# Kernel tuning notes

Hardware: AMD Instinct MI355X
Metric: run time of the kernel (lower is better)

Reference implementation:

```python
import jax, jax.numpy as jnp
import numpy as np

B = 4194304  # number of sequential rows


def setup_inputs() -> dict:
    key = jax.random.key(0)
    k1, k2, k3, k4 = jax.random.split(key, 4)
    x = jax.random.normal(k1, (B, 1, 3), dtype=jnp.float32)
    # nn.Linear(3, 3) params
    lim = 1.0 / np.sqrt(3.0)
    W = jax.random.uniform(k2, (3, 3), minval=-lim, maxval=lim, dtype=jnp.float32)
    b = jax.random.uniform(k3, (3,), minval=-lim, maxval=lim, dtype=jnp.float32)
    # FastNetwork init: (-1-1)*rand([3,1]) + 1  -> uniform in [-1, 1]
    net0 = jax.random.uniform(k4, (3, 1), minval=-1.0, maxval=1.0, dtype=jnp.float32)
    return {"x": x, "W": W, "b": b, "net0": net0}


def reference(x, W, b, net0):
    # x: [B,1,3]; W: [3,3]; b: [3]; net0: [3,1]
    xi = x[:, 0, :]                      # [B,3]
    # Updater: per-row Linear(3,3) -- batched as one matmul
    updates = xi @ W.T + b               # [B,3]

    def step(net, inp):
        x_row, u = inp                   # x_row: [3], u: [3]
        # 1/(1+exp(-10*(net + update - 0.5))) == sigmoid(10*(net + update - 0.5))
        net = jax.nn.sigmoid(10.0 * (net + u[:, None] - 0.5))  # [3,1]
        pred = x_row @ net               # [1]
        return net, pred

    _, preds = jax.lax.scan(step, net0, (xi, updates))
    return preds                         # [B,1]
```

## Files before the change

### kernel.cpp

```cpp
#include <hip/hip_runtime.h>


#if __has_builtin(__builtin_amdgcn_exp2f)
#define EXP2F(v) __builtin_amdgcn_exp2f(v)
#else
#define EXP2F(v) __expf(0.6931471805599453f * (v))
#endif

namespace {
constexpr int   BTOT   = 4194304;
constexpr int   CHUNK  = 16;
constexpr int   BLOCK  = 256;
constexpr int   BSTEPS = BLOCK * CHUNK;
constexpr int   WARM   = 32;
constexpr int   GRID   = BTOT / BSTEPS;
constexpr float KEXP   = -14.426950408889634f;
constexpr float EPS    = 1e-6f;
}

#define CVALS(X0, X1, X2)                                                     \
  const float c0 = fmaf(kw00, (X0), fmaf(kw01, (X1), fmaf(kw02, (X2), kb0)));  \
  const float c1 = fmaf(kw10, (X0), fmaf(kw11, (X1), fmaf(kw12, (X2), kb1)));  \
  const float c2 = fmaf(kw20, (X0), fmaf(kw21, (X1), fmaf(kw22, (X2), kb2)));

#define SIG(N, C) __builtin_amdgcn_rcpf(1.0f + EXP2F(fmaf(KEXP, (N), (C))))

#define US(X0, X1, X2)                                                        \
  do {                                                                        \
    CVALS(X0, X1, X2)                                                         \
    lo0 = SIG(lo0, c0); hi0 = SIG(hi0, c0);                                   \
    lo1 = SIG(lo1, c1); hi1 = SIG(hi1, c1);                                   \
    lo2 = SIG(lo2, c2); hi2 = SIG(hi2, c2);                                   \
  } while (0)

#define SS(X0, X1, X2)                                                        \
  do {                                                                        \
    CVALS(X0, X1, X2)                                                         \
    m0 = SIG(m0, c0); m1 = SIG(m1, c1); m2 = SIG(m2, c2);                     \
  } while (0)

#define MS(IDX, X0, X1, X2)                                                   \
  do {                                                                        \
    CVALS(X0, X1, X2)                                                         \
    m0 = SIG(m0, c0); m1 = SIG(m1, c1); m2 = SIG(m2, c2);                     \
    pr[(IDX)] = fmaf((X0), m0, fmaf((X1), m1, (X2) * m2));                    \
  } while (0)

__global__ __launch_bounds__(BLOCK, 4) void Updater_65395172049297_kernel(
    const float* __restrict__ x, const float* __restrict__ W,
    const float* __restrict__ bv, const float* __restrict__ n0v,
    float* __restrict__ out)
{
    const float kw00 = KEXP * W[0], kw01 = KEXP * W[1], kw02 = KEXP * W[2];
    const float kw10 = KEXP * W[3], kw11 = KEXP * W[4], kw12 = KEXP * W[5];
    const float kw20 = KEXP * W[6], kw21 = KEXP * W[7], kw22 = KEXP * W[8];
    const float kb0 = KEXP * (bv[0] - 0.5f);
    const float kb1 = KEXP * (bv[1] - 0.5f);
    const float kb2 = KEXP * (bv[2] - 0.5f);
    const float n00 = n0v[0], n01 = n0v[1], n02 = n0v[2];

    const long start = (long)blockIdx.x * BSTEPS + (long)threadIdx.x * CHUNK;
    const int  wl    = (int)((start < (long)WARM) ? start : (long)WARM);
    const bool exact = (start - wl) == 0;
    const int  gw    = wl >> 2;

    const float4* wp = reinterpret_cast<const float4*>(x + 3 * (start - wl));

    float lo0, lo1, lo2, hi0, hi1, hi2, m0, m1, m2;
    bool  conv = false;
    int   g    = 0;

    if (exact) {
        m0 = n00; m1 = n01; m2 = n02; conv = true;
    } else {
        lo0 = lo1 = lo2 = 0.0f; hi0 = hi1 = hi2 = 1.0f;
        float4 A = wp[0], B4 = wp[1], C4 = wp[2];
        while (g < gw) {
            const float4 An = wp[3 * g + 3], Bn = wp[3 * g + 4], Cn = wp[3 * g + 5];
            US(A.x, A.y, A.z);
            US(A.w, B4.x, B4.y);
            US(B4.z, B4.w, C4.x);
            US(C4.y, C4.z, C4.w);
            ++g;
            conv = ((hi0 - lo0) < EPS) & ((hi1 - lo1) < EPS) & ((hi2 - lo2) < EPS);
            if (__all(conv)) break;
            A = An; B4 = Bn; C4 = Cn;
        }
        if (conv) { m0 = 0.5f * (lo0 + hi0); m1 = 0.5f * (lo1 + hi1); m2 = 0.5f * (lo2 + hi2); }
    }

    if (conv) {
        for (; g < gw; ++g) {
            const float4 a4 = wp[3 * g], b4 = wp[3 * g + 1], c4 = wp[3 * g + 2];
            SS(a4.x, a4.y, a4.z);
            SS(a4.w, b4.x, b4.y);
            SS(b4.z, b4.w, c4.x);
            SS(c4.y, c4.z, c4.w);
        }
    } else {
        for (int at = 1; at < 10 && !conv; ++at) {
            long wl2 = (long)WARM << (2 * at);
            long bgn = start - wl2;
            bool ex2 = (bgn <= 0);
            if (ex2) bgn = 0;
            if (ex2) { lo0 = hi0 = n00; lo1 = hi1 = n01; lo2 = hi2 = n02; }
            else     { lo0 = lo1 = lo2 = 0.0f; hi0 = hi1 = hi2 = 1.0f; }
            const float4* bp = reinterpret_cast<const float4*>(x + 3 * bgn);
            const long ng = (start - bgn) >> 2;
            for (long q = 0; q < ng; ++q) {
                const float4 a4 = bp[3 * q], b4 = bp[3 * q + 1], c4 = bp[3 * q + 2];
                US(a4.x, a4.y, a4.z);
                US(a4.w, b4.x, b4.y);
                US(b4.z, b4.w, c4.x);
                US(c4.y, c4.z, c4.w);
            }
            conv = ex2 || (((hi0 - lo0) < EPS) & ((hi1 - lo1) < EPS) & ((hi2 - lo2) < EPS));
        }
        m0 = 0.5f * (lo0 + hi0); m1 = 0.5f * (lo1 + hi1); m2 = 0.5f * (lo2 + hi2);
    }

    const float4* mp = reinterpret_cast<const float4*>(x + 3 * start);
    float pr[CHUNK];
#pragma unroll
    for (int q = 0; q < CHUNK / 4; ++q) {
        const float4 a4 = mp[3 * q], b4 = mp[3 * q + 1], c4 = mp[3 * q + 2];
        MS(4 * q + 0, a4.x, a4.y, a4.z);
        MS(4 * q + 1, a4.w, b4.x, b4.y);
        MS(4 * q + 2, b4.z, b4.w, c4.x);
        MS(4 * q + 3, c4.y, c4.z, c4.w);
    }

    float4* op = reinterpret_cast<float4*>(out + start);
#pragma unroll
    for (int i = 0; i < CHUNK / 4; ++i)
        op[i] = make_float4(pr[4 * i + 0], pr[4 * i + 1], pr[4 * i + 2], pr[4 * i + 3]);
}

extern "C" void kernel_launch(void* const* d_in, const int* in_sizes, int n_in,
                              void* d_out, int out_size, void* d_ws, size_t ws_size,
                              hipStream_t stream) {
    const float* x   = (const float*)d_in[0];
    const float* W   = (const float*)d_in[1];
    const float* bv  = (const float*)d_in[2];
    const float* n0v = (const float*)d_in[3];
    float*       out = (float*)d_out;
    Updater_65395172049297_kernel<<<GRID, BLOCK, 0, stream>>>(x, W, bv, n0v, out);
}
```

Before: 117.4 us.

## Source warm-up rows from neighbor lanes via ds_bpermute instead of global reloads

Each thread now loads its own 16 rows once into registers. During the 32-step warm-up it pulls the preceding rows from lanes one or two positions lower using ds_bpermute, rather than re-reading the overlapping window from global memory. The first lanes of each wavefront, which have no lower neighbor, read their warm-up rows from a small shared-memory buffer filled before a block barrier. The main pass reuses the register copy of the rows, and the warm-up is fully unrolled with predication for the first wavefront. In exchange it adds register pressure from the 48-float array, cross-lane shuffles, a __syncthreads, and more complex unrolled control flow.

Measured after the change: 103.3 us. 12.0% less time.

```diff
diff --git a/kernel.cpp b/kernel.cpp
--- a/kernel.cpp
+++ b/kernel.cpp
@@ -18,39 +18,104 @@
 constexpr float EPS    = 1e-6f;
 }
 
-#define CVALS(X0, X1, X2)                                                     \
-  const float c0 = fmaf(kw00, (X0), fmaf(kw01, (X1), fmaf(kw02, (X2), kb0)));  \
-  const float c1 = fmaf(kw10, (X0), fmaf(kw11, (X1), fmaf(kw12, (X2), kb1)));  \
-  const float c2 = fmaf(kw20, (X0), fmaf(kw21, (X1), fmaf(kw22, (X2), kb2)));
+#define CVALS(X0_, X1_, X2_)                                                   \
+  const float c0 = fmaf(kw00, (X0_), fmaf(kw01, (X1_), fmaf(kw02, (X2_), kb0))); \
+  const float c1 = fmaf(kw10, (X0_), fmaf(kw11, (X1_), fmaf(kw12, (X2_), kb1))); \
+  const float c2 = fmaf(kw20, (X0_), fmaf(kw21, (X1_), fmaf(kw22, (X2_), kb2)));
 
 #define SIG(N, C) __builtin_amdgcn_rcpf(1.0f + EXP2F(fmaf(KEXP, (N), (C))))
 
-#define US(X0, X1, X2)                                                        \
-  do {                                                                        \
-    CVALS(X0, X1, X2)                                                         \
-    lo0 = SIG(lo0, c0); hi0 = SIG(hi0, c0);                                   \
-    lo1 = SIG(lo1, c1); hi1 = SIG(hi1, c1);                                   \
-    lo2 = SIG(lo2, c2); hi2 = SIG(hi2, c2);                                   \
+#define PULL(VAL_, AD_)                                                        \
+  __int_as_float(__builtin_amdgcn_ds_bpermute((AD_), __float_as_int(VAL_)))
+
+#define WSTEP_FETCH(S_)                                                        \
+  float X0, X1, X2;                                                            \
+  {                                                                            \
+    const int ad_ = ((S_) < 16) ? a2 : a1;                                     \
+    X0 = PULL(fx[3 * ((S_) & 15) + 0], ad_);                                   \
+    X1 = PULL(fx[3 * ((S_) & 15) + 1], ad_);                                   \
+    X2 = PULL(fx[3 * ((S_) & 15) + 2], ad_);                                   \
+    if (lane < (((S_) < 16) ? 2 : 1)) {                                        \
+      const float4 wv = wbuf[w][lane * 16 + (S_)];                             \
+      X0 = wv.x; X1 = wv.y; X2 = wv.z;                                         \
+    }                                                                          \
+  }
+
+#define WSTEP_DUAL(S_, PRED_)                                                  \
+  {                                                                            \
+    WSTEP_FETCH(S_)                                                            \
+    CVALS(X0, X1, X2)                                                          \
+    const float a0_ = SIG(lo0, c0), b0_ = SIG(hi0, c0);                        \
+    const float a1_ = SIG(lo1, c1), b1_ = SIG(hi1, c1);                        \
+    const float a2_ = SIG(lo2, c2), b2_ = SIG(hi2, c2);                        \
+    if (PRED_) {                                                               \
+      const bool kp_ = (S_) >= smin;                                           \
+      lo0 = kp_ ? a0_ : lo0; hi0 = kp_ ? b0_ : hi0;                            \
+      lo1 = kp_ ? a1_ : lo1; hi1 = kp_ ? b1_ : hi1;                            \
+      lo2 = kp_ ? a2_ : lo2; hi2 = kp_ ? b2_ : hi2;                            \
+    } else {                                                                   \
+      lo0 = a0_; hi0 = b0_; lo1 = a1_; hi1 = b1_; lo2 = a2_; hi2 = b2_;        \
+    }                                                                          \
+  }
+
+#define WSTEP_SNG(S_, PRED_)                                                   \
+  {                                                                            \
+    WSTEP_FETCH(S_)                                                            \
+    CVALS(X0, X1, X2)                                                          \
+    const float t0_ = SIG(m0, c0), t1_ = SIG(m1, c1), t2_ = SIG(m2, c2);       \
+    if (PRED_) {                                                               \
+      const bool kp_ = (S_) >= smin;                                           \
+      m0 = kp_ ? t0_ : m0; m1 = kp_ ? t1_ : m1; m2 = kp_ ? t2_ : m2;           \
+    } else {                                                                   \
+      m0 = t0_; m1 = t1_; m2 = t2_;                                            \
+    }                                                                          \
+  }
+
+#define WARM_GROUP(G_, PRED_)                                                  \
+  if (!single) {                                                               \
+    WSTEP_DUAL(4 * (G_) + 0, PRED_)                                            \
+    WSTEP_DUAL(4 * (G_) + 1, PRED_)                                            \
+    WSTEP_DUAL(4 * (G_) + 2, PRED_)                                            \
+    WSTEP_DUAL(4 * (G_) + 3, PRED_)                                            \
+    conv = ((hi0 - lo0) < EPS) & ((hi1 - lo1) < EPS) & ((hi2 - lo2) < EPS);    \
+    if (__all(conv)) {                                                         \
+      m0 = 0.5f * (lo0 + hi0); m1 = 0.5f * (lo1 + hi1); m2 = 0.5f * (lo2 + hi2); \
+      single = true;                                                           \
+    }                                                                          \
+  } else {                                                                     \
+    WSTEP_SNG(4 * (G_) + 0, PRED_)                                             \
+    WSTEP_SNG(4 * (G_) + 1, PRED_)                                             \
+    WSTEP_SNG(4 * (G_) + 2, PRED_)                                             \
+    WSTEP_SNG(4 * (G_) + 3, PRED_)                                             \
+  }
+
+#define WARM_ALL(PRED_)                                                        \
+  WARM_GROUP(0, PRED_) WARM_GROUP(1, PRED_) WARM_GROUP(2, PRED_)               \
+  WARM_GROUP(3, PRED_) WARM_GROUP(4, PRED_) WARM_GROUP(5, PRED_)               \
+  WARM_GROUP(6, PRED_) WARM_GROUP(7, PRED_)
+
+#define US(X0_, X1_, X2_)                                                      \
+  do {                                                                         \
+    CVALS(X0_, X1_, X2_)                                                       \
+    lo0 = SIG(lo0, c0); hi0 = SIG(hi0, c0);                                    \
+    lo1 = SIG(lo1, c1); hi1 = SIG(hi1, c1);                                    \
+    lo2 = SIG(lo2, c2); hi2 = SIG(hi2, c2);                                    \
   } while (0)
 
-#define SS(X0, X1, X2)                                                        \
-  do {                                                                        \
-    CVALS(X0, X1, X2)                                                         \
-    m0 = SIG(m0, c0); m1 = SIG(m1, c1); m2 = SIG(m2, c2);                     \
-  } while (0)
-
-#define MS(IDX, X0, X1, X2)                                                   \
-  do {                                                                        \
-    CVALS(X0, X1, X2)                                                         \
-    m0 = SIG(m0, c0); m1 = SIG(m1, c1); m2 = SIG(m2, c2);                     \
-    pr[(IDX)] = fmaf((X0), m0, fmaf((X1), m1, (X2) * m2));                    \
-  } while (0)
+#define MS(P_, X0_, X1_, X2_)                                                  \
+  {                                                                            \
+    CVALS(X0_, X1_, X2_)                                                       \
+    m0 = SIG(m0, c0); m1 = SIG(m1, c1); m2 = SIG(m2, c2);                      \
+    P_ = fmaf((X0_), m0, fmaf((X1_), m1, (X2_) * m2));                         \
+  }
 
 __global__ __launch_bounds__(BLOCK, 4) void Updater_65395172049297_kernel(
     const float* __restrict__ x, const float* __restrict__ W,
     const float* __restrict__ bv, const float* __restrict__ n0v,
     float* __restrict__ out)
 {
+    __shared__ float4 wbuf[BLOCK / 64][WARM];
+
     const float kw00 = KEXP * W[0], kw01 = KEXP * W[1], kw02 = KEXP * W[2];
     const float kw10 = KEXP * W[3], kw11 = KEXP * W[4], kw12 = KEXP * W[5];
     const float kw20 = KEXP * W[6], kw21 = KEXP * W[7], kw22 = KEXP * W[8];
@@ -59,81 +124,84 @@
     const float kb2 = KEXP * (bv[2] - 0.5f);
     const float n00 = n0v[0], n01 = n0v[1], n02 = n0v[2];
 
-    const long start = (long)blockIdx.x * BSTEPS + (long)threadIdx.x * CHUNK;
-    const int  wl    = (int)((start < (long)WARM) ? start : (long)WARM);
-    const bool exact = (start - wl) == 0;
-    const int  gw    = wl >> 2;
-
-    const float4* wp = reinterpret_cast<const float4*>(x + 3 * (start - wl));
-
-    float lo0, lo1, lo2, hi0, hi1, hi2, m0, m1, m2;
-    bool  conv = false;
-    int   g    = 0;
-
-    if (exact) {
-        m0 = n00; m1 = n01; m2 = n02; conv = true;
-    } else {
-        lo0 = lo1 = lo2 = 0.0f; hi0 = hi1 = hi2 = 1.0f;
-        float4 A = wp[0], B4 = wp[1], C4 = wp[2];
-        while (g < gw) {
-            const float4 An = wp[3 * g + 3], Bn = wp[3 * g + 4], Cn = wp[3 * g + 5];
-            US(A.x, A.y, A.z);
-            US(A.w, B4.x, B4.y);
-            US(B4.z, B4.w, C4.x);
-            US(C4.y, C4.z, C4.w);
-            ++g;
-            conv = ((hi0 - lo0) < EPS) & ((hi1 - lo1) < EPS) & ((hi2 - lo2) < EPS);
-            if (__all(conv)) break;
-            A = An; B4 = Bn; C4 = Cn;
+    const int  lane  = threadIdx.x & 63;
+    const int  w     = threadIdx.x >> 6;
+    const long S     = (long)blockIdx.x * BSTEPS;
+    const long start = S + (long)threadIdx.x * CHUNK;
+
+    const int a2 = ((lane >= 2) ? (lane - 2) : lane) << 2;
+    const int a1 = ((lane >= 1) ? (lane - 1) : lane) << 2;
+
+    float fx[48];
+    {
+        const float4* mp = reinterpret_cast<const float4*>(x + 3 * start);
+#pragma unroll
+        for (int i = 0; i < 12; ++i) {
+            const float4 v = mp[i];
+            fx[4 * i + 0] = v.x; fx[4 * i + 1] = v.y;
+            fx[4 * i + 2] = v.z; fx[4 * i + 3] = v.w;
         }
-        if (conv) { m0 = 0.5f * (lo0 + hi0); m1 = 0.5f * (lo1 + hi1); m2 = 0.5f * (lo2 + hi2); }
-    }
-
-    if (conv) {
-        for (; g < gw; ++g) {
-            const float4 a4 = wp[3 * g], b4 = wp[3 * g + 1], c4 = wp[3 * g + 2];
-            SS(a4.x, a4.y, a4.z);
-            SS(a4.w, b4.x, b4.y);
-            SS(b4.z, b4.w, c4.x);
-            SS(c4.y, c4.z, c4.w);
+    }
+
+    {
+        const long wbase = S + (long)w * (64 * CHUNK);
+        if (lane < WARM) {
+            long sstep = wbase - WARM + lane;
+            if (sstep < 0) sstep = 0;
+            const float* xp = x + 3 * sstep;
+            wbuf[w][lane] = make_float4(xp[0], xp[1], xp[2], 0.0f);
         }
-    } else {
-        for (int at = 1; at < 10 && !conv; ++at) {
-            long wl2 = (long)WARM << (2 * at);
-            long bgn = start - wl2;
-            bool ex2 = (bgn <= 0);
-            if (ex2) bgn = 0;
-            if (ex2) { lo0 = hi0 = n00; lo1 = hi1 = n01; lo2 = hi2 = n02; }
-            else     { lo0 = lo1 = lo2 = 0.0f; hi0 = hi1 = hi2 = 1.0f; }
-            const float4* bp = reinterpret_cast<const float4*>(x + 3 * bgn);
-            const long ng = (start - bgn) >> 2;
-            for (long q = 0; q < ng; ++q) {
-                const float4 a4 = bp[3 * q], b4 = bp[3 * q + 1], c4 = bp[3 * q + 2];
-                US(a4.x, a4.y, a4.z);
-                US(a4.w, b4.x, b4.y);
-                US(b4.z, b4.w, c4.x);
-                US(c4.y, c4.z, c4.w);
+    }
+    __syncthreads();
+
+    const bool exact = (start <= (long)WARM);
+    const int  smin  = exact ? (int)(WARM - (int)start) : 0;
+    const bool special = (blockIdx.x == 0) && (w == 0);
+
+    float lo0, lo1, lo2, hi0, hi1, hi2;
+    if (exact) { lo0 = hi0 = n00; lo1 = hi1 = n01; lo2 = hi2 = n02; }
+    else       { lo0 = lo1 = lo2 = 0.0f; hi0 = hi1 = hi2 = 1.0f; }
+
+    bool  conv = false, single = false;
+    float m0 = n00, m1 = n01, m2 = n02;
+
+    if (special) { WARM_ALL(true) } else { WARM_ALL(false) }
+
+    if (!single) {
+        if (!conv) {
+            for (int at = 1; at < 10 && !conv; ++at) {
+                long wl2 = (long)WARM << (2 * at);
+                long bgn = start - wl2;
+                bool ex2 = (bgn <= 0);
+                if (ex2) bgn = 0;
+                if (ex2) { lo0 = hi0 = n00; lo1 = hi1 = n01; lo2 = hi2 = n02; }
+                else     { lo0 = lo1 = lo2 = 0.0f; hi0 = hi1 = hi2 = 1.0f; }
+                const float4* bp = reinterpret_cast<const float4*>(x + 3 * bgn);
+                const long ng = (start - bgn) >> 2;
+                for (long q = 0; q < ng; ++q) {
+                    const float4 a4 = bp[3 * q], b4 = bp[3 * q + 1], c4 = bp[3 * q + 2];
+                    US(a4.x, a4.y, a4.z);
+                    US(a4.w, b4.x, b4.y);
+                    US(b4.z, b4.w, c4.x);
+                    US(c4.y, c4.z, c4.w);
+                }
+                conv = ex2 || (((hi0 - lo0) < EPS) & ((hi1 - lo1) < EPS) &
+                               ((hi2 - lo2) < EPS));
             }
-            conv = ex2 || (((hi0 - lo0) < EPS) & ((hi1 - lo1) < EPS) & ((hi2 - lo2) < EPS));
         }
         m0 = 0.5f * (lo0 + hi0); m1 = 0.5f * (lo1 + hi1); m2 = 0.5f * (lo2 + hi2);
     }
 
-    const float4* mp = reinterpret_cast<const float4*>(x + 3 * start);
-    float pr[CHUNK];
-#pragma unroll
-    for (int q = 0; q < CHUNK / 4; ++q) {
-        const float4 a4 = mp[3 * q], b4 = mp[3 * q + 1], c4 = mp[3 * q + 2];
-        MS(4 * q + 0, a4.x, a4.y, a4.z);
-        MS(4 * q + 1, a4.w, b4.x, b4.y);
-        MS(4 * q + 2, b4.z, b4.w, c4.x);
-        MS(4 * q + 3, c4.y, c4.z, c4.w);
-    }
-
     float4* op = reinterpret_cast<float4*>(out + start);
 #pragma unroll
-    for (int i = 0; i < CHUNK / 4; ++i)
-        op[i] = make_float4(pr[4 * i + 0], pr[4 * i + 1], pr[4 * i + 2], pr[4 * i + 3]);
+    for (int q = 0; q < 4; ++q) {
+        float p0, p1, p2, p3;
+        MS(p0, fx[12 * q + 0], fx[12 * q + 1], fx[12 * q + 2]);
+        MS(p1, fx[12 * q + 3], fx[12 * q + 4], fx[12 * q + 5]);
+        MS(p2, fx[12 * q + 6], fx[12 * q + 7], fx[12 * q + 8]);
+        MS(p3, fx[12 * q + 9], fx[12 * q + 10], fx[12 * q + 11]);
+        op[q] = make_float4(p0, p1, p2, p3);
+    }
 }
 
 extern "C" void kernel_launch(void* const* d_in, const int* in_sizes, int n_in,
```
